# Optimization experiments

Measured on AMD Instinct MI355X. Metric: run time of the kernel, lower is better.

## Reference

```python
import jax, jax.numpy as jnp
import numpy as np

B, N, C, H = 8, 2048, 2048, 16


def setup_inputs() -> dict:
    key = jax.random.key(0)
    k1, k2, k3, k4 = jax.random.split(key, 4)
    x = jax.random.normal(k1, (B, N, C), dtype=jnp.float32)
    W_attn = jax.random.normal(k2, (C, C), dtype=jnp.float32) * 0.02
    W_proj = jax.random.normal(k3, (C, C), dtype=jnp.float32) * 0.02
    temp = jnp.ones((H, 1), dtype=jnp.float32)
    denom_bias = jax.random.normal(k4, (H, N, 1), dtype=jnp.float32) * 0.01
    return {"x": x, "W_attn": W_attn, "W_proj": W_proj, "temp": temp, "denom_bias": denom_bias}


def reference(x, W_attn, W_proj, temp, denom_bias):
    # x: (B, N, C); dropout layers are identity in eval mode.
    b, n, c = x.shape
    h = temp.shape[0]
    d = c // h
    eps = jnp.float32(jnp.finfo(jnp.float16).eps)  # fp16 eps used by the original

    # w: (B, H, N, D)
    w = jnp.einsum('bnc,oc->bno', x, W_attn).reshape(b, n, h, d).transpose(0, 2, 1, 3)
    w_sq = w * w

    # cumulative per-feature normalization along sequence
    denom = jnp.maximum(jnp.cumsum(w_sq, axis=2), eps)              # (B,H,N,D)
    w_normed = w_sq / denom + denom_bias[None, :, :n, :]            # (B,H,N,D)

    tmp = jnp.sum(w_normed, axis=-1) * temp[None]                   # (B,H,N), temp (H,1) broadcasts over N
    Pi = jax.nn.softmax(tmp, axis=1)                                # softmax over heads

    # second cumulative scan weighted by Pi
    dots = jnp.cumsum(w_sq * Pi[..., None], axis=2) / (jnp.cumsum(Pi, axis=-1) + eps)[..., None]
    attn = 1.0 / (1.0 + dots)                                       # (B,H,N,D)

    y = -(w * Pi[..., None]) * attn                                 # (B,H,N,D)
    y = y.transpose(0, 2, 1, 3).reshape(b, n, c)                    # (B,N,C)
    return jnp.einsum('bnc,oc->bno', y, W_proj)
```

## Files before the change

### kernel.cpp

```cpp
#include <hip/hip_runtime.h>
#include <math.h>

typedef _Float16 f16;
typedef f16 f16x8 __attribute__((ext_vector_type(8)));
typedef float f32x4 __attribute__((ext_vector_type(4)));

#define EPS_F16 0.0009765625f


__global__ __launch_bounds__(256) void k_cast8h(const float* __restrict__ in,
                                                f16* __restrict__ out,
                                                long long n8) {
  long long i = (long long)blockIdx.x * blockDim.x + threadIdx.x;
  if (i >= n8) return;
  const float4* in4 = (const float4*)in;
  float4 a = in4[i * 2];
  float4 b = in4[i * 2 + 1];
  f16x8 o;
  o[0] = (f16)a.x; o[1] = (f16)a.y; o[2] = (f16)a.z; o[3] = (f16)a.w;
  o[4] = (f16)b.x; o[5] = (f16)b.y; o[6] = (f16)b.z; o[7] = (f16)b.w;
  *(f16x8*)(out + i * 8) = o;
}

__device__ __forceinline__ void gl2lds16(const void* g, void* l) {
  __builtin_amdgcn_global_load_lds(
      (const __attribute__((address_space(1))) void*)g,
      (__attribute__((address_space(3))) void*)l, 16, 0, 0);
}

__device__ __forceinline__ void drain_barrier() {
  asm volatile("s_waitcnt vmcnt(0) lgkmcnt(0)" ::: "memory");
  __builtin_amdgcn_sched_barrier(0);
  __syncthreads();
}

template <int MODE>
__global__ __launch_bounds__(512, 2) void gemm256(const f16* __restrict__ A,
                                                  const f16* __restrict__ Bm,
                                                  float* __restrict__ Cout,
                                                  float* __restrict__ psum) {
  constexpr int K = 2048;
  __shared__ alignas(16) char lds[131072];
  const int t = threadIdx.x;
  const int lane = t & 63;
  const int wid = t >> 6;
  const int wm = wid >> 2;
  const int wn = wid & 3;
  const size_t bm = (size_t)blockIdx.y * 256;
  const size_t bn = (size_t)blockIdx.x * 256;

  size_t aOff[4], bOff[4];
  int sp[4];
#pragma unroll
  for (int j = 0; j < 4; ++j) {
    int sr = j * 64 + (t >> 7) * 16 + ((t & 63) >> 2);
    int sc = ((t >> 6) & 1) * 32 + (((t & 3) * 8) ^ (((t >> 5) & 1) << 4));
    sp[j] = j * 8192 + t * 16;
    aOff[j] = (bm + (size_t)sr) * K + sc;
    bOff[j] = (bn + (size_t)sr) * K + sc;
  }

  const int lbyte = (((lane & 15) * 64 + (lane >> 4) * 16) ^ ((lane & 8) << 2));

  f32x4 acc[8][4] = {};

#pragma unroll
  for (int j = 0; j < 4; ++j) {
    gl2lds16(A + aOff[j], lds + sp[j]);
    gl2lds16(Bm + bOff[j], lds + 32768 + sp[j]);
  }
  drain_barrier();

  int s = 0;
  for (int kt = 0; kt < K / 64; ++kt) {
    if (kt + 1 < K / 64) {
      const int ns = s ^ 1;
      const size_t ko = (size_t)(kt + 1) * 64;
#pragma unroll
      for (int j = 0; j < 4; ++j) {
        gl2lds16(A + aOff[j] + ko, lds + ns * 65536 + sp[j]);
        gl2lds16(Bm + bOff[j] + ko, lds + ns * 65536 + 32768 + sp[j]);
      }
    }
    const char* Ab = lds + s * 65536 + wm * 16384 + lbyte;
    const char* Bb = lds + s * 65536 + 32768 + wn * 8192 + lbyte;
    f16x8 bfrag[4][2];
#pragma unroll
    for (int q = 0; q < 4; ++q) {
      if (q == 0) {
#pragma unroll
        for (int fj = 0; fj < 4; ++fj)
#pragma unroll
          for (int k2 = 0; k2 < 2; ++k2)
            bfrag[fj][k2] = *(const f16x8*)(Bb + (fj * 2 + k2) * 1024);
      }
      f16x8 afrag[2][2];
#pragma unroll
      for (int mi = 0; mi < 2; ++mi)
#pragma unroll
        for (int k2 = 0; k2 < 2; ++k2)
          afrag[mi][k2] = *(const f16x8*)(Ab + ((q * 2 + mi) * 2 + k2) * 1024);
#pragma unroll
      for (int mi = 0; mi < 2; ++mi)
#pragma unroll
        for (int fj = 0; fj < 4; ++fj)
#pragma unroll
          for (int k2 = 0; k2 < 2; ++k2)
            acc[q * 2 + mi][fj] = __builtin_amdgcn_mfma_f32_16x16x32_f16(
                afrag[mi][k2], bfrag[fj][k2], acc[q * 2 + mi][fj], 0, 0, 0);
    }
    drain_barrier();
    s ^= 1;
  }

  const int col = lane & 15;
  const int rb = (lane >> 4) * 4;
#pragma unroll
  for (int fi = 0; fi < 8; ++fi)
#pragma unroll
    for (int fj = 0; fj < 4; ++fj)
#pragma unroll
      for (int r = 0; r < 4; ++r) {
        size_t gr = bm + wm * 128 + fi * 16 + rb + r;
        size_t gc = bn + wn * 64 + fj * 16 + col;
        float v = acc[fi][fj][r];
        if constexpr (MODE == 0) {
          Cout[gr * 2048 + gc] = v;
        } else {
          Cout[(((gr >> 11) * 16 + (gc >> 7)) * 2048 + (gr & 2047)) * 128 +
               (gc & 127)] = v;
        }
      }
  if constexpr (MODE == 1) {
#pragma unroll
    for (int fj = 0; fj < 4; ++fj) {
      float ss = 0.f;
#pragma unroll
      for (int fi = 0; fi < 8; ++fi)
#pragma unroll
        for (int r = 0; r < 4; ++r) ss += acc[fi][fj][r] * acc[fi][fj][r];
      ss += __shfl_xor(ss, 16);
      ss += __shfl_xor(ss, 32);
      if (lane < 16) {
        int b = (int)(bm >> 11);
        int h = (int)(bn >> 7) + (wn >> 1);
        int chunk = (int)((bm & 2047) >> 7) + wm;
        int d = (wn & 1) * 64 + fj * 16 + lane;
        psum[(((size_t)(b * 16 + h)) * 16 + chunk) * 128 + d] = ss;
      }
    }
  }
}

__global__ __launch_bounds__(256) void k_prefix(float* __restrict__ psum) {
  int idx = blockIdx.x * 256 + threadIdx.x;
  int bh = idx >> 7, d = idx & 127;
  float run = 0.f;
#pragma unroll
  for (int c = 0; c < 16; ++c) {
    size_t o = ((size_t)bh * 16 + c) * 128 + d;
    float v = psum[o];
    psum[o] = run;
    run += v;
  }
}

__device__ __forceinline__ int swz(int i, int j) { return i * 128 + (j ^ (i & 31)); }

__global__ __launch_bounds__(128) void k_tmp(const float* __restrict__ w,
                                             const float* __restrict__ pre,
                                             const float* __restrict__ dbias,
                                             const float* __restrict__ temp,
                                             float* __restrict__ tmp) {
  __shared__ float ratio[128 * 128];
  int blk = blockIdx.x;
  int bh = blk >> 4, chunk = blk & 15;
  int h = bh & 15;
  int d = threadIdx.x;
  const float* base =
      w + ((size_t)bh * 2048 + (size_t)chunk * 128) * 128 + d;
  float cum = pre[((size_t)bh * 16 + chunk) * 128 + d];
  for (int i = 0; i < 128; ++i) {
    float v = base[(size_t)i * 128];
    float sq = v * v;
    cum += sq;
    float dn = fmaxf(cum, EPS_F16);
    ratio[swz(i, d)] = sq / dn;
  }
  __syncthreads();
  float s = 0.f;
#pragma unroll 8
  for (int j = 0; j < 128; ++j) s += ratio[swz(d, j)];
  int n = chunk * 128 + d;
  tmp[(size_t)bh * 2048 + n] = (s + 128.f * dbias[h * 2048 + n]) * temp[h];
}

__global__ __launch_bounds__(256) void k_softmax(const float* __restrict__ tmp,
                                                 float* __restrict__ Pi) {
  int idx = blockIdx.x * 256 + threadIdx.x;
  int b = idx >> 11, n = idx & 2047;
  float v[16];
  float mx = -1e30f;
#pragma unroll
  for (int h = 0; h < 16; ++h) {
    v[h] = tmp[((size_t)(b * 16 + h)) * 2048 + n];
    mx = fmaxf(mx, v[h]);
  }
  float s = 0.f;
#pragma unroll
  for (int h = 0; h < 16; ++h) {
    v[h] = expf(v[h] - mx);
    s += v[h];
  }
  float inv = 1.f / s;
#pragma unroll
  for (int h = 0; h < 16; ++h)
    Pi[((size_t)(b * 16 + h)) * 2048 + n] = v[h] * inv;
}

__global__ __launch_bounds__(128) void k_partial2(const float* __restrict__ w,
                                                  const float* __restrict__ Pi,
                                                  float* __restrict__ psum,
                                                  float* __restrict__ pisum) {
  int blk = blockIdx.x;
  int bh = blk >> 4, chunk = blk & 15;
  int d = threadIdx.x;
  const float* base =
      w + ((size_t)bh * 2048 + (size_t)chunk * 128) * 128 + d;
  const float* pib = Pi + (size_t)bh * 2048 + (size_t)chunk * 128;
  float s = 0.f, sp = 0.f;
#pragma unroll 4
  for (int i = 0; i < 128; ++i) {
    float p = pib[i];
    float v = base[(size_t)i * 128];
    s += v * v * p;
    sp += p;
  }
  psum[(size_t)blk * 128 + d] = s;
  if (d == 0) pisum[blk] = sp;
}

__global__ __launch_bounds__(128) void k_prefix_pi(float* __restrict__ pisum) {
  int bh = threadIdx.x;
  float run = 0.f;
#pragma unroll
  for (int c = 0; c < 16; ++c) {
    int o = bh * 16 + c;
    float v = pisum[o];
    pisum[o] = run;
    run += v;
  }
}

__global__ __launch_bounds__(128) void k_y(const float* __restrict__ w,
                                           const float* __restrict__ Pi,
                                           const float* __restrict__ pre2,
                                           const float* __restrict__ piPre,
                                           f16* __restrict__ yout) {
  int blk = blockIdx.x;
  int bh = blk >> 4, chunk = blk & 15;
  int b = bh >> 4, h = bh & 15;
  int d = threadIdx.x;
  const float* base =
      w + ((size_t)bh * 2048 + (size_t)chunk * 128) * 128 + d;
  const float* pib = Pi + (size_t)bh * 2048 + (size_t)chunk * 128;
  float cum = pre2[((size_t)bh * 16 + chunk) * 128 + d];
  float cpi = piPre[bh * 16 + chunk];
  for (int i = 0; i < 128; ++i) {
    float p = pib[i];
    float v = base[(size_t)i * 128];
    cum += v * v * p;
    cpi += p;
    float dots = cum / (cpi + EPS_F16);
    float attn = 1.f / (1.f + dots);
    float y = -(v * p) * attn;
    int n = chunk * 128 + i;
    yout[((size_t)(b * 2048 + n)) * 2048 + h * 128 + d] = (f16)y;
  }
}

extern "C" void kernel_launch(void* const* d_in, const int* in_sizes, int n_in,
                              void* d_out, int out_size, void* d_ws, size_t ws_size,
                              hipStream_t stream) {
  const float* x     = (const float*)d_in[0];
  const float* Wa    = (const float*)d_in[1];
  const float* Wp    = (const float*)d_in[2];
  const float* temp  = (const float*)d_in[3];
  const float* dbias = (const float*)d_in[4];
  float* out = (float*)d_out;

  char* ws = (char*)d_ws;
  constexpr size_t OFF_W   = 0;
  constexpr size_t OFF_XH  = 134217728;
  constexpr size_t OFF_WAH = OFF_XH + 67108864;
  constexpr size_t OFF_WPB = OFF_WAH + 8388608;
  constexpr size_t OFF_TMP = OFF_WPB + 8388608;
  constexpr size_t OFF_PI  = OFF_TMP + 2097152;
  constexpr size_t OFF_PS  = OFF_PI + 2097152;
  constexpr size_t OFF_PIS = OFF_PS + 1048576;

  float* w    = (float*)(ws + OFF_W);
  f16*   xh   = (f16*)(ws + OFF_XH);
  f16*   Wah  = (f16*)(ws + OFF_WAH);
  f16*   Wpb  = (f16*)(ws + OFF_WPB);
  float* tmp  = (float*)(ws + OFF_TMP);
  float* Pi   = (float*)(ws + OFF_PI);
  float* psum = (float*)(ws + OFF_PS);
  float* pis  = (float*)(ws + OFF_PIS);

  k_cast8h<<<16384, 256, 0, stream>>>(x, xh, 4194304LL);
  k_cast8h<<<2048, 256, 0, stream>>>(Wa, Wah, 524288LL);
  k_cast8h<<<2048, 256, 0, stream>>>(Wp, Wpb, 524288LL);

  gemm256<1><<<dim3(8, 64), 512, 0, stream>>>(xh, Wah, w, psum);

  k_prefix<<<64, 256, 0, stream>>>(psum);
  k_tmp<<<2048, 128, 0, stream>>>(w, psum, dbias, temp, tmp);

  k_softmax<<<64, 256, 0, stream>>>(tmp, Pi);

  k_partial2<<<2048, 128, 0, stream>>>(w, Pi, psum, pis);
  k_prefix<<<64, 256, 0, stream>>>(psum);
  k_prefix_pi<<<1, 128, 0, stream>>>(pis);
  k_y<<<2048, 128, 0, stream>>>(w, Pi, psum, pis, xh);

  gemm256<0><<<dim3(8, 64), 512, 0, stream>>>(xh, Wpb, out, nullptr);
}
```

Before: 450.8 us.

## Store intermediate projection in fp16 and remap GEMM block order

The first GEMM now writes the head-major intermediate w as fp16 instead of fp32, halving its write traffic and the read traffic of the three scan kernels that consume it. The sum-of-squares partials are computed from the rounded values so they stay consistent with what downstream kernels read. Separately, GEMM blocks are remapped so consecutive launched blocks walk down M for a fixed N column, which changes L2 reuse of the weight and activation tiles. The fp16 storage adds rounding error to w in exchange for the bandwidth saving.

```diff
diff --git a/kernel.cpp b/kernel.cpp
--- a/kernel.cpp
+++ b/kernel.cpp
@@ -38,6 +38,7 @@
 __global__ __launch_bounds__(512, 2) void gemm256(const f16* __restrict__ A,
                                                   const f16* __restrict__ Bm,
                                                   float* __restrict__ Cout,
+                                                  f16* __restrict__ Wout,
                                                   float* __restrict__ psum) {
   constexpr int K = 2048;
   __shared__ alignas(16) char lds[131072];
@@ -46,8 +47,11 @@
   const int wid = t >> 6;
   const int wm = wid >> 2;
   const int wn = wid & 3;
-  const size_t bm = (size_t)blockIdx.y * 256;
-  const size_t bn = (size_t)blockIdx.x * 256;
+
+  const int lin = blockIdx.y * 8 + blockIdx.x;
+  const int logical = (lin & 7) * 64 + (lin >> 3);
+  const size_t bm = (size_t)(logical >> 3) * 256;
+  const size_t bn = (size_t)(logical & 7) * 256;
 
   size_t aOff[4], bOff[4];
   int sp[4];
@@ -115,30 +119,33 @@
 
   const int col = lane & 15;
   const int rb = (lane >> 4) * 4;
-#pragma unroll
-  for (int fi = 0; fi < 8; ++fi)
-#pragma unroll
-    for (int fj = 0; fj < 4; ++fj)
-#pragma unroll
-      for (int r = 0; r < 4; ++r) {
-        size_t gr = bm + wm * 128 + fi * 16 + rb + r;
-        size_t gc = bn + wn * 64 + fj * 16 + col;
-        float v = acc[fi][fj][r];
-        if constexpr (MODE == 0) {
-          Cout[gr * 2048 + gc] = v;
-        } else {
-          Cout[(((gr >> 11) * 16 + (gc >> 7)) * 2048 + (gr & 2047)) * 128 +
-               (gc & 127)] = v;
+  if constexpr (MODE == 0) {
+#pragma unroll
+    for (int fi = 0; fi < 8; ++fi)
+#pragma unroll
+      for (int fj = 0; fj < 4; ++fj)
+#pragma unroll
+        for (int r = 0; r < 4; ++r) {
+          size_t gr = bm + wm * 128 + fi * 16 + rb + r;
+          size_t gc = bn + wn * 64 + fj * 16 + col;
+          Cout[gr * 2048 + gc] = acc[fi][fj][r];
         }
-      }
-  if constexpr (MODE == 1) {
+  } else {
 #pragma unroll
     for (int fj = 0; fj < 4; ++fj) {
       float ss = 0.f;
 #pragma unroll
       for (int fi = 0; fi < 8; ++fi)
 #pragma unroll
-        for (int r = 0; r < 4; ++r) ss += acc[fi][fj][r] * acc[fi][fj][r];
+        for (int r = 0; r < 4; ++r) {
+          size_t gr = bm + wm * 128 + fi * 16 + rb + r;
+          size_t gc = bn + wn * 64 + fj * 16 + col;
+          f16 q = (f16)acc[fi][fj][r];
+          Wout[(((gr >> 11) * 16 + (gc >> 7)) * 2048 + (gr & 2047)) * 128 +
+               (gc & 127)] = q;
+          float qf = (float)q;
+          ss += qf * qf;
+        }
       ss += __shfl_xor(ss, 16);
       ss += __shfl_xor(ss, 32);
       if (lane < 16) {
@@ -167,7 +174,7 @@
 
 __device__ __forceinline__ int swz(int i, int j) { return i * 128 + (j ^ (i & 31)); }
 
-__global__ __launch_bounds__(128) void k_tmp(const float* __restrict__ w,
+__global__ __launch_bounds__(128) void k_tmp(const f16* __restrict__ w,
                                              const float* __restrict__ pre,
                                              const float* __restrict__ dbias,
                                              const float* __restrict__ temp,
@@ -177,11 +184,11 @@
   int bh = blk >> 4, chunk = blk & 15;
   int h = bh & 15;
   int d = threadIdx.x;
-  const float* base =
+  const f16* base =
       w + ((size_t)bh * 2048 + (size_t)chunk * 128) * 128 + d;
   float cum = pre[((size_t)bh * 16 + chunk) * 128 + d];
   for (int i = 0; i < 128; ++i) {
-    float v = base[(size_t)i * 128];
+    float v = (float)base[(size_t)i * 128];
     float sq = v * v;
     cum += sq;
     float dn = fmaxf(cum, EPS_F16);
@@ -218,21 +225,21 @@
     Pi[((size_t)(b * 16 + h)) * 2048 + n] = v[h] * inv;
 }
 
-__global__ __launch_bounds__(128) void k_partial2(const float* __restrict__ w,
+__global__ __launch_bounds__(128) void k_partial2(const f16* __restrict__ w,
                                                   const float* __restrict__ Pi,
                                                   float* __restrict__ psum,
                                                   float* __restrict__ pisum) {
   int blk = blockIdx.x;
   int bh = blk >> 4, chunk = blk & 15;
   int d = threadIdx.x;
-  const float* base =
+  const f16* base =
       w + ((size_t)bh * 2048 + (size_t)chunk * 128) * 128 + d;
   const float* pib = Pi + (size_t)bh * 2048 + (size_t)chunk * 128;
   float s = 0.f, sp = 0.f;
 #pragma unroll 4
   for (int i = 0; i < 128; ++i) {
     float p = pib[i];
-    float v = base[(size_t)i * 128];
+    float v = (float)base[(size_t)i * 128];
     s += v * v * p;
     sp += p;
   }
@@ -252,7 +259,7 @@
   }
 }
 
-__global__ __launch_bounds__(128) void k_y(const float* __restrict__ w,
+__global__ __launch_bounds__(128) void k_y(const f16* __restrict__ w,
                                            const float* __restrict__ Pi,
                                            const float* __restrict__ pre2,
                                            const float* __restrict__ piPre,
@@ -261,14 +268,14 @@
   int bh = blk >> 4, chunk = blk & 15;
   int b = bh >> 4, h = bh & 15;
   int d = threadIdx.x;
-  const float* base =
+  const f16* base =
       w + ((size_t)bh * 2048 + (size_t)chunk * 128) * 128 + d;
   const float* pib = Pi + (size_t)bh * 2048 + (size_t)chunk * 128;
   float cum = pre2[((size_t)bh * 16 + chunk) * 128 + d];
   float cpi = piPre[bh * 16 + chunk];
   for (int i = 0; i < 128; ++i) {
     float p = pib[i];
-    float v = base[(size_t)i * 128];
+    float v = (float)base[(size_t)i * 128];
     cum += v * v * p;
     cpi += p;
     float dots = cum / (cpi + EPS_F16);
@@ -291,7 +298,7 @@
 
   char* ws = (char*)d_ws;
   constexpr size_t OFF_W   = 0;
-  constexpr size_t OFF_XH  = 134217728;
+  constexpr size_t OFF_XH  = 67108864;
   constexpr size_t OFF_WAH = OFF_XH + 67108864;
   constexpr size_t OFF_WPB = OFF_WAH + 8388608;
   constexpr size_t OFF_TMP = OFF_WPB + 8388608;
@@ -299,7 +306,7 @@
   constexpr size_t OFF_PS  = OFF_PI + 2097152;
   constexpr size_t OFF_PIS = OFF_PS + 1048576;
 
-  float* w    = (float*)(ws + OFF_W);
+  f16*   w    = (f16*)(ws + OFF_W);
   f16*   xh   = (f16*)(ws + OFF_XH);
   f16*   Wah  = (f16*)(ws + OFF_WAH);
   f16*   Wpb  = (f16*)(ws + OFF_WPB);
@@ -312,7 +319,7 @@
   k_cast8h<<<2048, 256, 0, stream>>>(Wa, Wah, 524288LL);
   k_cast8h<<<2048, 256, 0, stream>>>(Wp, Wpb, 524288LL);
 
-  gemm256<1><<<dim3(8, 64), 512, 0, stream>>>(xh, Wah, w, psum);
+  gemm256<1><<<dim3(8, 64), 512, 0, stream>>>(xh, Wah, nullptr, w, psum);
 
   k_prefix<<<64, 256, 0, stream>>>(psum);
   k_tmp<<<2048, 128, 0, stream>>>(w, psum, dbias, temp, tmp);
@@ -324,5 +331,5 @@
   k_prefix_pi<<<1, 128, 0, stream>>>(pis);
   k_y<<<2048, 128, 0, stream>>>(w, Pi, psum, pis, xh);
 
-  gemm256<0><<<dim3(8, 64), 512, 0, stream>>>(xh, Wpb, out, nullptr);
-}
+  gemm256<0><<<dim3(8, 64), 512, 0, stream>>>(xh, Wpb, out, nullptr, nullptr);
+}
```

New measurement: 445.5 us. About the same (-1.2%).
